# Performance work log

Hardware: AMD Instinct MI355X
Metric: run time of the kernel (lower is better)

## Reference

```python
import jax, jax.numpy as jnp
import numpy as np

R = 8                 # level-0 resolution (voxels per block side)
STRIDE = 8**3 + 2**3  # 520: total voxels per block across levels [8,2]
OFFSET = 0            # level-0 offset into the per-block voxel buffer
V = 0.01              # level-0 voxel size
G = 32                # dense block-grid side (stand-in for sparse hashmap domain)
CAP = 20000           # hashmap capacity (allocated blocks)
N = 2_000_000         # query points
F = 5                 # feature dim: 1 sdf + 1 weight + 3 rgb

_CORNERS = jnp.array([[i, j, k] for i in (0, 1) for j in (0, 1) for k in (0, 1)], dtype=jnp.int32)  # [8,3]


def setup_inputs() -> dict:
    key = jax.random.key(0)
    k1, k2, k3 = jax.random.split(key, 3)
    block_size = V * R
    # query points inside the active domain [0, G*block_size)
    x = jax.random.uniform(k1, (N, 3), dtype=jnp.float32) * (G * block_size)
    feat_params = jax.random.normal(k2, (CAP, STRIDE, F), dtype=jnp.float32) * 0.1
    # hashmap stand-in: unique block indices for CAP of the G^3 block coords, -1 = empty
    perm = jax.random.permutation(k3, G ** 3)
    block_table = jnp.where(perm < CAP, perm, -1).reshape(G, G, G).astype(jnp.int32)
    return {"x": x, "feat_params": feat_params, "block_table": block_table}


def reference(x, feat_params, block_table):
    # sparse multi-res voxel feature gather + trilinear interp + analytic grad (level 0)
    u = x / V                                  # global voxel-space coords
    xi = jnp.floor(u).astype(jnp.int32)        # [N,3] base voxel
    frac = u - xi                              # [N,3] trilinear fractions
    gv = xi[:, None, :] + _CORNERS[None]       # [N,8,3] corner voxel coords
    bc = jnp.floor_divide(gv, R)               # block coords per corner
    lc = gv - bc * R                           # in-block voxel coords
    inb = jnp.all((bc >= 0) & (bc < G), axis=-1)           # [N,8]
    bcs = jnp.clip(bc, 0, G - 1)
    bidx = block_table[bcs[..., 0], bcs[..., 1], bcs[..., 2]]  # [N,8] hashmap lookup
    found = inb & (bidx >= 0)
    masks = jnp.all(found, axis=1)             # [N] all 8 corners allocated
    bsafe = jnp.maximum(bidx, 0)
    vidx = OFFSET + (lc[..., 0] * R + lc[..., 1]) * R + lc[..., 2]  # [N,8]
    f = feat_params[bsafe, vidx]               # [N,8,F] irregular gather
    # trilinear weights and their spatial derivatives
    w01 = jnp.stack([1.0 - frac, frac], axis=-1)                        # [N,3,2]
    P = w01[:, jnp.arange(3)[None, :], _CORNERS]                        # [N,8,3]
    S = (2 * _CORNERS - 1).astype(x.dtype)                              # [8,3] d(w)/d(u)
    w = P[..., 0] * P[..., 1] * P[..., 2]                               # [N,8]
    dw = jnp.stack([S[None, :, 0] * P[..., 1] * P[..., 2],
                    P[..., 0] * S[None, :, 1] * P[..., 2],
                    P[..., 0] * P[..., 1] * S[None, :, 2]], axis=-1)    # [N,8,3]
    m = masks.astype(x.dtype)
    feats = jnp.einsum('nc,ncf->nf', w, f) * m[:, None]                 # [N,F]
    dfeats_dx = jnp.einsum('ncd,ncf->nfd', dw, f) * (m[:, None, None] / V)  # [N,F,3]
    return feats, dfeats_dx, masks
```

## Files before the change

kernel.cpp:

```cpp
#include <hip/hip_runtime.h>
#include <math.h>

#define NPTS 2000000
#define GG 32
#define FF 5
#define BLK 256

typedef float v4f __attribute__((ext_vector_type(4)));
typedef float v2f __attribute__((ext_vector_type(2)));

__global__ __launch_bounds__(256) void hashgrid_kernel(
    const float* __restrict__ x,
    const float* __restrict__ feat,
    const int* __restrict__ btab,
    float* __restrict__ out)
{
    __shared__ float smem[5120];
    const int tid  = threadIdx.x;
    const int bid  = blockIdx.x;
    const int base = bid * BLK;
    const int cnt  = min(BLK, NPTS - base);

    {
        const float4* xin = (const float4*)(x + (size_t)base * 3);
        float4* s4 = (float4*)smem;
        int nf4 = (cnt * 3) >> 2;
        for (int i = tid; i < nf4; i += BLK) s4[i] = xin[i];
    }
    __syncthreads();

    float x0 = 0.f, x1 = 0.f, x2 = 0.f;
    if (tid < cnt) { x0 = smem[tid*3+0]; x1 = smem[tid*3+1]; x2 = smem[tid*3+2]; }
    __syncthreads();

    float accf[5] = {0,0,0,0,0};
    float adx[5]  = {0,0,0,0,0};
    float ady[5]  = {0,0,0,0,0};
    float adz[5]  = {0,0,0,0,0};
    float mval = 0.f;

    if (tid < cnt) {
        float u0 = x0 * 100.0f, u1 = x1 * 100.0f, u2 = x2 * 100.0f;
        float fl0 = floorf(u0), fl1 = floorf(u1), fl2 = floorf(u2);
        int xi0 = (int)fl0, xi1 = (int)fl1, xi2 = (int)fl2;
        float fr0 = u0 - fl0, fr1 = u1 - fl1, fr2 = u2 - fl2;

        int vidx[8];
        #pragma unroll
        for (int c = 0; c < 8; ++c) {
            int i = (c >> 2) & 1, j = (c >> 1) & 1, k = c & 1;
            vidx[c] = (((xi0 + i) & 7) * 8 + ((xi1 + j) & 7)) * 8 + ((xi2 + k) & 7);
        }

        const bool fx = (xi0 & 7) == 7;
        const bool fy = (xi1 & 7) == 7;
        const bool cz = (xi2 & 7) == 7;
        const int ncross = (int)fx + (int)fy + (int)cz;
        const int blo = ((xi0 >> 3) * GG + (xi1 >> 3)) * GG + (xi2 >> 3);

        int bv0, bv1, bvm[8];
        int dsel = 0; bool hi_ok = true; bool inb[8];
        if (ncross == 0) {
            asm volatile("global_load_dword %0, %1, off"
                         : "=&v"(bv0) : "v"(btab + blo));
        } else if (ncross == 1) {
            dsel       = fx ? 4 : (fy ? 2 : 1);
            int stride = fx ? GG * GG : (fy ? GG : 1);
            int bcoord = fx ? (xi0 >> 3) : (fy ? (xi1 >> 3) : (xi2 >> 3));
            hi_ok      = (bcoord + 1) < GG;
            asm volatile("global_load_dword %0, %1, off"
                         : "=&v"(bv0) : "v"(btab + blo));
            asm volatile("global_load_dword %0, %1, off"
                         : "=&v"(bv1) : "v"(btab + blo + (hi_ok ? stride : 0)));
        } else {
            #pragma unroll
            for (int c = 0; c < 8; ++c) {
                int i = (c >> 2) & 1, j = (c >> 1) & 1, k = c & 1;
                int g0 = xi0 + i, g1 = xi1 + j, g2 = xi2 + k;
                int b0 = g0 >> 3, b1 = g1 >> 3, b2 = g2 >> 3;
                inb[c] = ((unsigned)b0 < GG) & ((unsigned)b1 < GG) & ((unsigned)b2 < GG);
                int c0 = min(max(b0,0),GG-1), c1 = min(max(b1,0),GG-1), c2 = min(max(b2,0),GG-1);
                asm volatile("global_load_dword %0, %1, off"
                             : "=&v"(bvm[c]) : "v"(btab + ((c0 * GG + c1) * GG + c2)));
            }
        }

        bool ok = false;
        int offs[8];
        if (ncross == 0) {
            asm volatile("s_waitcnt vmcnt(0)" : "+v"(bv0));
            __builtin_amdgcn_sched_barrier(0);
            ok = bv0 >= 0;
            int bo = max(bv0, 0) * 520;
            #pragma unroll
            for (int c = 0; c < 8; ++c) offs[c] = bo + vidx[c];
        } else if (ncross == 1) {
            asm volatile("s_waitcnt vmcnt(0)" : "+v"(bv0), "+v"(bv1));
            __builtin_amdgcn_sched_barrier(0);
            ok = hi_ok & (bv0 >= 0) & (bv1 >= 0);
            int blo_s = max(bv0, 0) * 520;
            int bhi_s = max(bv1, 0) * 520;
            #pragma unroll
            for (int c = 0; c < 8; ++c)
                offs[c] = ((c & dsel) ? bhi_s : blo_s) + vidx[c];
        } else {
            asm volatile("s_waitcnt vmcnt(0)"
                         : "+v"(bvm[0]), "+v"(bvm[1]), "+v"(bvm[2]), "+v"(bvm[3]),
                           "+v"(bvm[4]), "+v"(bvm[5]), "+v"(bvm[6]), "+v"(bvm[7]));
            __builtin_amdgcn_sched_barrier(0);
            ok = true;
            #pragma unroll
            for (int c = 0; c < 8; ++c) {
                ok &= inb[c] & (bvm[c] >= 0);
                offs[c] = max(bvm[c], 0) * 520 + vidx[c];
            }
        }

        if (ok) {
            mval = 1.f;
            float p0[2] = {1.f - fr0, fr0};
            float p1[2] = {1.f - fr1, fr1};
            float p2[2] = {1.f - fr2, fr2};

            v4f A[4], B[4]; v2f C[4];
            v4f q[8]; float t[8];
            if (!cz) {
                #pragma unroll
                for (int p = 0; p < 4; ++p) {
                    const float* fp = feat + (size_t)offs[p*2] * 5;
                    asm volatile("global_load_dwordx4 %0, %1, off"
                                 : "=&v"(A[p]) : "v"(fp));
                    asm volatile("global_load_dwordx4 %0, %1, off offset:16"
                                 : "=&v"(B[p]) : "v"(fp));
                    asm volatile("global_load_dwordx2 %0, %1, off offset:32"
                                 : "=&v"(C[p]) : "v"(fp));
                }
            } else {
                #pragma unroll
                for (int c = 0; c < 8; ++c) {
                    const float* fp = feat + (size_t)offs[c] * 5;
                    asm volatile("global_load_dwordx4 %0, %1, off"
                                 : "=&v"(q[c]) : "v"(fp));
                    asm volatile("global_load_dword %0, %1, off offset:16"
                                 : "=&v"(t[c]) : "v"(fp));
                }
            }

            if (!cz) {
                asm volatile("s_waitcnt vmcnt(0)"
                             : "+v"(A[0]), "+v"(A[1]), "+v"(A[2]), "+v"(A[3]),
                               "+v"(B[0]), "+v"(B[1]), "+v"(B[2]), "+v"(B[3]),
                               "+v"(C[0]), "+v"(C[1]), "+v"(C[2]), "+v"(C[3]));
                __builtin_amdgcn_sched_barrier(0);
                #pragma unroll
                for (int p = 0; p < 4; ++p) {
                    int i = (p >> 1) & 1, j = p & 1;
                    float wi = p0[i], wj = p1[j];
                    float si = i ? 1.f : -1.f;
                    float sj = j ? 1.f : -1.f;
                    float wij = wi * wj;
                    float dxy = si * wj;
                    float dyx = wi * sj;
                    {
                        float wk = p2[0];
                        float w = wij * wk, dwx = dxy * wk, dwy = dyx * wk, dwz = -wij;
                        float vv[5] = {A[p][0], A[p][1], A[p][2], A[p][3], B[p][0]};
                        #pragma unroll
                        for (int f = 0; f < 5; ++f) {
                            float v = vv[f];
                            accf[f] += w   * v;
                            adx[f]  += dwx * v;
                            ady[f]  += dwy * v;
                            adz[f]  += dwz * v;
                        }
                    }
                    {
                        float wk = p2[1];
                        float w = wij * wk, dwx = dxy * wk, dwy = dyx * wk, dwz = wij;
                        float vv[5] = {B[p][1], B[p][2], B[p][3], C[p][0], C[p][1]};
                        #pragma unroll
                        for (int f = 0; f < 5; ++f) {
                            float v = vv[f];
                            accf[f] += w   * v;
                            adx[f]  += dwx * v;
                            ady[f]  += dwy * v;
                            adz[f]  += dwz * v;
                        }
                    }
                }
            } else {
                asm volatile("s_waitcnt vmcnt(0)"
                             : "+v"(q[0]), "+v"(q[1]), "+v"(q[2]), "+v"(q[3]),
                               "+v"(q[4]), "+v"(q[5]), "+v"(q[6]), "+v"(q[7]),
                               "+v"(t[0]), "+v"(t[1]), "+v"(t[2]), "+v"(t[3]),
                               "+v"(t[4]), "+v"(t[5]), "+v"(t[6]), "+v"(t[7]));
                __builtin_amdgcn_sched_barrier(0);
                #pragma unroll
                for (int c = 0; c < 8; ++c) {
                    int i = (c >> 2) & 1, j = (c >> 1) & 1, k = c & 1;
                    float wi = p0[i], wj = p1[j], wk = p2[k];
                    float si = i ? 1.f : -1.f;
                    float sj = j ? 1.f : -1.f;
                    float sk = k ? 1.f : -1.f;
                    float w   = wi * wj * wk;
                    float dwx = si * wj * wk;
                    float dwy = wi * sj * wk;
                    float dwz = wi * wj * sk;
                    float vv[5] = {q[c][0], q[c][1], q[c][2], q[c][3], t[c]};
                    #pragma unroll
                    for (int f = 0; f < 5; ++f) {
                        float v = vv[f];
                        accf[f] += w   * v;
                        adx[f]  += dwx * v;
                        ady[f]  += dwy * v;
                        adz[f]  += dwz * v;
                    }
                }
            }
        }
    }

    if (tid < cnt) {
        float* fs = smem + tid * 5;
        #pragma unroll
        for (int f = 0; f < 5; ++f) fs[f] = accf[f];
        float* ds = smem + 1280 + tid * 15;
        #pragma unroll
        for (int f = 0; f < 5; ++f) {
            ds[f*3+0] = adx[f] * 100.0f;
            ds[f*3+1] = ady[f] * 100.0f;
            ds[f*3+2] = adz[f] * 100.0f;
        }
        out[(size_t)NPTS * 20 + base + tid] = mval;
    }
    __syncthreads();

    {
        const float4* s4 = (const float4*)smem;
        float4* o = (float4*)(out + (size_t)base * 5);
        int nf4 = (cnt * 5) >> 2;
        for (int i = tid; i < nf4; i += BLK) o[i] = s4[i];
    }
    {
        const float4* s4 = (const float4*)(smem + 1280);
        float4* o = (float4*)(out + (size_t)NPTS * 5 + (size_t)base * 15);
        int nf4 = (cnt * 15) >> 2;
        for (int i = tid; i < nf4; i += BLK) o[i] = s4[i];
    }
}

extern "C" void kernel_launch(void* const* d_in, const int* in_sizes, int n_in,
                              void* d_out, int out_size, void* d_ws, size_t ws_size,
                              hipStream_t stream) {
    const float* x    = (const float*)d_in[0];
    const float* feat = (const float*)d_in[1];
    const int*   btab = (const int*)d_in[2];
    float* out = (float*)d_out;
    int blocks = (NPTS + BLK - 1) / BLK;
    hashgrid_kernel<<<blocks, BLK, 0, stream>>>(x, feat, btab, out);
}
```

Baseline: 399.3 us.

## Cooperative wave-level feature gather through LDS with uniform dwordx4 loads

```diff
diff --git a/kernel.cpp b/kernel.cpp
--- a/kernel.cpp
+++ b/kernel.cpp
@@ -3,11 +3,9 @@
 
 #define NPTS 2000000
 #define GG 32
-#define FF 5
 #define BLK 256
 
 typedef float v4f __attribute__((ext_vector_type(4)));
-typedef float v2f __attribute__((ext_vector_type(2)));
 
 __global__ __launch_bounds__(256) void hashgrid_kernel(
     const float* __restrict__ x,
@@ -15,7 +13,8 @@
     const int* __restrict__ btab,
     float* __restrict__ out)
 {
-    __shared__ float smem[5120];
+    __shared__ float smem[12800];
+    int* ofsl = (int*)&smem[10496];
     const int tid  = threadIdx.x;
     const int bid  = blockIdx.x;
     const int base = bid * BLK;
@@ -31,19 +30,15 @@
 
     float x0 = 0.f, x1 = 0.f, x2 = 0.f;
     if (tid < cnt) { x0 = smem[tid*3+0]; x1 = smem[tid*3+1]; x2 = smem[tid*3+2]; }
-    __syncthreads();
-
-    float accf[5] = {0,0,0,0,0};
-    float adx[5]  = {0,0,0,0,0};
-    float ady[5]  = {0,0,0,0,0};
-    float adz[5]  = {0,0,0,0,0};
-    float mval = 0.f;
-
+
+    float fr0 = 0.f, fr1 = 0.f, fr2 = 0.f;
+    bool ok = false;
+    int offs[8] = {0,0,0,0,0,0,0,0};
     if (tid < cnt) {
         float u0 = x0 * 100.0f, u1 = x1 * 100.0f, u2 = x2 * 100.0f;
         float fl0 = floorf(u0), fl1 = floorf(u1), fl2 = floorf(u2);
         int xi0 = (int)fl0, xi1 = (int)fl1, xi2 = (int)fl2;
-        float fr0 = u0 - fl0, fr1 = u1 - fl1, fr2 = u2 - fl2;
+        fr0 = u0 - fl0; fr1 = u1 - fl1; fr2 = u2 - fl2;
 
         int vidx[8];
         #pragma unroll
@@ -85,8 +80,6 @@
             }
         }
 
-        bool ok = false;
-        int offs[8];
         if (ncross == 0) {
             asm volatile("s_waitcnt vmcnt(0)" : "+v"(bv0));
             __builtin_amdgcn_sched_barrier(0);
@@ -115,110 +108,86 @@
                 offs[c] = max(bvm[c], 0) * 520 + vidx[c];
             }
         }
-
-        if (ok) {
-            mval = 1.f;
-            float p0[2] = {1.f - fr0, fr0};
-            float p1[2] = {1.f - fr1, fr1};
-            float p2[2] = {1.f - fr2, fr2};
-
-            v4f A[4], B[4]; v2f C[4];
-            v4f q[8]; float t[8];
-            if (!cz) {
-                #pragma unroll
-                for (int p = 0; p < 4; ++p) {
-                    const float* fp = feat + (size_t)offs[p*2] * 5;
-                    asm volatile("global_load_dwordx4 %0, %1, off"
-                                 : "=&v"(A[p]) : "v"(fp));
-                    asm volatile("global_load_dwordx4 %0, %1, off offset:16"
-                                 : "=&v"(B[p]) : "v"(fp));
-                    asm volatile("global_load_dwordx2 %0, %1, off offset:32"
-                                 : "=&v"(C[p]) : "v"(fp));
-                }
+        if (!ok) {
+            #pragma unroll
+            for (int c = 0; c < 8; ++c) offs[c] = 0;
+        }
+    }
+
+    #pragma unroll
+    for (int c = 0; c < 8; ++c) ofsl[tid*9 + c] = offs[c];
+    __syncthreads();
+
+    {
+        const int lane  = tid & 63;
+        const int wbase = tid & ~63;
+        const int sub   = lane >> 4;
+        const int cc    = (lane >> 1) & 7;
+        const int ss    = lane & 1;
+        int Pv[16]; int ov[16];
+        #pragma unroll
+        for (int r = 0; r < 16; ++r) {
+            Pv[r] = wbase + r * 4 + sub;
+            ov[r] = ofsl[Pv[r] * 9 + cc];
+        }
+        v4f q[16];
+        #pragma unroll
+        for (int r = 0; r < 16; ++r) {
+            const float* fp = feat + (size_t)((unsigned)ov[r] * 5u + (unsigned)ss);
+            asm volatile("global_load_dwordx4 %0, %1, off"
+                         : "=&v"(q[r]) : "v"(fp));
+        }
+        asm volatile("s_waitcnt vmcnt(0)"
+                     : "+v"(q[0]), "+v"(q[1]), "+v"(q[2]), "+v"(q[3]),
+                       "+v"(q[4]), "+v"(q[5]), "+v"(q[6]), "+v"(q[7]),
+                       "+v"(q[8]), "+v"(q[9]), "+v"(q[10]), "+v"(q[11]),
+                       "+v"(q[12]), "+v"(q[13]), "+v"(q[14]), "+v"(q[15]));
+        __builtin_amdgcn_sched_barrier(0);
+        #pragma unroll
+        for (int r = 0; r < 16; ++r) {
+            float* fb = &smem[Pv[r] * 41 + cc * 5];
+            if (ss == 0) {
+                fb[0] = q[r][0]; fb[1] = q[r][1]; fb[2] = q[r][2]; fb[3] = q[r][3];
             } else {
-                #pragma unroll
-                for (int c = 0; c < 8; ++c) {
-                    const float* fp = feat + (size_t)offs[c] * 5;
-                    asm volatile("global_load_dwordx4 %0, %1, off"
-                                 : "=&v"(q[c]) : "v"(fp));
-                    asm volatile("global_load_dword %0, %1, off offset:16"
-                                 : "=&v"(t[c]) : "v"(fp));
-                }
-            }
-
-            if (!cz) {
-                asm volatile("s_waitcnt vmcnt(0)"
-                             : "+v"(A[0]), "+v"(A[1]), "+v"(A[2]), "+v"(A[3]),
-                               "+v"(B[0]), "+v"(B[1]), "+v"(B[2]), "+v"(B[3]),
-                               "+v"(C[0]), "+v"(C[1]), "+v"(C[2]), "+v"(C[3]));
-                __builtin_amdgcn_sched_barrier(0);
-                #pragma unroll
-                for (int p = 0; p < 4; ++p) {
-                    int i = (p >> 1) & 1, j = p & 1;
-                    float wi = p0[i], wj = p1[j];
-                    float si = i ? 1.f : -1.f;
-                    float sj = j ? 1.f : -1.f;
-                    float wij = wi * wj;
-                    float dxy = si * wj;
-                    float dyx = wi * sj;
-                    {
-                        float wk = p2[0];
-                        float w = wij * wk, dwx = dxy * wk, dwy = dyx * wk, dwz = -wij;
-                        float vv[5] = {A[p][0], A[p][1], A[p][2], A[p][3], B[p][0]};
-                        #pragma unroll
-                        for (int f = 0; f < 5; ++f) {
-                            float v = vv[f];
-                            accf[f] += w   * v;
-                            adx[f]  += dwx * v;
-                            ady[f]  += dwy * v;
-                            adz[f]  += dwz * v;
-                        }
-                    }
-                    {
-                        float wk = p2[1];
-                        float w = wij * wk, dwx = dxy * wk, dwy = dyx * wk, dwz = wij;
-                        float vv[5] = {B[p][1], B[p][2], B[p][3], C[p][0], C[p][1]};
-                        #pragma unroll
-                        for (int f = 0; f < 5; ++f) {
-                            float v = vv[f];
-                            accf[f] += w   * v;
-                            adx[f]  += dwx * v;
-                            ady[f]  += dwy * v;
-                            adz[f]  += dwz * v;
-                        }
-                    }
-                }
-            } else {
-                asm volatile("s_waitcnt vmcnt(0)"
-                             : "+v"(q[0]), "+v"(q[1]), "+v"(q[2]), "+v"(q[3]),
-                               "+v"(q[4]), "+v"(q[5]), "+v"(q[6]), "+v"(q[7]),
-                               "+v"(t[0]), "+v"(t[1]), "+v"(t[2]), "+v"(t[3]),
-                               "+v"(t[4]), "+v"(t[5]), "+v"(t[6]), "+v"(t[7]));
-                __builtin_amdgcn_sched_barrier(0);
-                #pragma unroll
-                for (int c = 0; c < 8; ++c) {
-                    int i = (c >> 2) & 1, j = (c >> 1) & 1, k = c & 1;
-                    float wi = p0[i], wj = p1[j], wk = p2[k];
-                    float si = i ? 1.f : -1.f;
-                    float sj = j ? 1.f : -1.f;
-                    float sk = k ? 1.f : -1.f;
-                    float w   = wi * wj * wk;
-                    float dwx = si * wj * wk;
-                    float dwy = wi * sj * wk;
-                    float dwz = wi * wj * sk;
-                    float vv[5] = {q[c][0], q[c][1], q[c][2], q[c][3], t[c]};
-                    #pragma unroll
-                    for (int f = 0; f < 5; ++f) {
-                        float v = vv[f];
-                        accf[f] += w   * v;
-                        adx[f]  += dwx * v;
-                        ady[f]  += dwy * v;
-                        adz[f]  += dwz * v;
-                    }
-                }
-            }
-        }
-    }
+                fb[4] = q[r][3];
+            }
+        }
+    }
+    __syncthreads();
+
+    float accf[5] = {0,0,0,0,0};
+    float adx[5]  = {0,0,0,0,0};
+    float ady[5]  = {0,0,0,0,0};
+    float adz[5]  = {0,0,0,0,0};
+    float mval = 0.f;
+    if (tid < cnt && ok) {
+        mval = 1.f;
+        float p0[2] = {1.f - fr0, fr0};
+        float p1[2] = {1.f - fr1, fr1};
+        float p2[2] = {1.f - fr2, fr2};
+        const float* myf = &smem[tid * 41];
+        #pragma unroll
+        for (int c = 0; c < 8; ++c) {
+            int i = (c >> 2) & 1, j = (c >> 1) & 1, k = c & 1;
+            float wi = p0[i], wj = p1[j], wk = p2[k];
+            float si = i ? 1.f : -1.f;
+            float sj = j ? 1.f : -1.f;
+            float sk = k ? 1.f : -1.f;
+            float w   = wi * wj * wk;
+            float dwx = si * wj * wk;
+            float dwy = wi * sj * wk;
+            float dwz = wi * wj * sk;
+            #pragma unroll
+            for (int f = 0; f < 5; ++f) {
+                float v = myf[c * 5 + f];
+                accf[f] += w   * v;
+                adx[f]  += dwx * v;
+                ady[f]  += dwy * v;
+                adz[f]  += dwz * v;
+            }
+        }
+    }
+    __syncthreads();
 
     if (tid < cnt) {
         float* fs = smem + tid * 5;
```

Measured after the change: 401.7 us. No clear change (+0.6%).
